# Optimization experiments

Measured on AMD Instinct MI355X. Metric: run time of the kernel, lower is better.

Reference implementation:

```python
import jax, jax.numpy as jnp
import numpy as np

B, SEQ, C, H, L = 2, 512, 768, 12, 6
OBS = ACT = GOAL = 64
MAXEP = 1000
D = C // H
T3 = 3 * SEQ  # stacked (z, state, action) tokens per timestep


def _ln(x, g, b):
    m = jnp.mean(x, -1, keepdims=True)
    v = jnp.mean((x - m) ** 2, -1, keepdims=True)
    return (x - m) * jax.lax.rsqrt(v + 1e-5) * g + b


def setup_inputs() -> dict:
    key = jax.random.key(0)
    it = iter(jax.random.split(key, 64))
    nrm = lambda shape, s=0.02: jax.random.normal(next(it), shape, jnp.float32) * s
    z = lambda *s: jnp.zeros(s, jnp.float32)
    o = lambda *s: jnp.ones(s, jnp.float32)
    return dict(
        states=jax.random.normal(next(it), (B, SEQ, OBS), jnp.float32),
        actions=jax.random.normal(next(it), (B, SEQ, ACT), jnp.float32),
        goals=jax.random.normal(next(it), (B, 1, GOAL), jnp.float32),
        traj_mask=jnp.ones((B, SEQ), bool),
        timesteps=jax.random.randint(next(it), (B, SEQ), 0, MAXEP),
        W_s=nrm((OBS, C)), b_s=z(C),
        W_a=nrm((ACT, C)), b_a=z(C),
        W_g=nrm((GOAL, C)), b_g=z(C),
        E_t=nrm((MAXEP, C)),
        ln0_g=o(C), ln0_b=z(C),
        Wq=nrm((L, C, C)), bq=z(L, C),
        Wk=nrm((L, C, C)), bk=z(L, C),
        Wv=nrm((L, C, C)), bv=z(L, C),
        Wp=nrm((L, C, C)), bp=z(L, C),
        ln1_g=o(L, C), ln1_b=z(L, C),
        W1=nrm((L, C, 4 * C)), b1=z(L, 4 * C),
        W2=nrm((L, 4 * C, C)), b2=z(L, C),
        ln2_g=o(L, C), ln2_b=z(L, C),
        W_ps=nrm((C, OBS)), b_ps=z(OBS),
        W_pa=nrm((C, ACT)), b_pa=z(ACT),
    )


def _forward(states, actions, goals, timesteps,
             W_s, b_s, W_a, b_a, W_g, b_g, E_t, ln0_g, ln0_b,
             Wq, bq, Wk, bk, Wv, bv, Wp, bp, ln1_g, ln1_b,
             W1, b1, W2, b2, ln2_g, ln2_b, W_ps, b_ps, W_pa, b_pa):
    te = E_t[timesteps]  # [B,SEQ,C] time embeddings (use_pe_as_timestep path)
    s_emb = states @ W_s + b_s + te
    a_emb = actions @ W_a + b_a + te
    g = jnp.broadcast_to(goals, (goals.shape[0], SEQ, goals.shape[2]))
    z_emb = g @ W_g + b_g + te  # GOAL_CONDITION path
    # interleave (z, s, a) per timestep -> [B, 3*SEQ, C]
    x = jnp.stack((z_emb, s_emb, a_emb), axis=2).reshape(states.shape[0], T3, C)
    x = _ln(x, ln0_g, ln0_b)
    mask = jnp.tril(jnp.ones((T3, T3), bool))
    scale = 1.0 / np.sqrt(D)
    for l in range(L):
        q = (x @ Wq[l] + bq[l]).reshape(-1, T3, H, D)
        k = (x @ Wk[l] + bk[l]).reshape(-1, T3, H, D)
        v = (x @ Wv[l] + bv[l]).reshape(-1, T3, H, D)
        sc = jnp.einsum('bqhd,bkhd->bhqk', q, k) * scale
        sc = jnp.where(mask, sc, -jnp.inf)
        w = jax.nn.softmax(sc, axis=-1)
        att = jnp.einsum('bhqk,bkhd->bqhd', w, v).reshape(-1, T3, C)
        x = x + att @ Wp[l] + bp[l]
        x = _ln(x, ln1_g[l], ln1_b[l])
        h = jax.nn.gelu(x @ W1[l] + b1[l], approximate=False)
        x = x + h @ W2[l] + b2[l]
        x = _ln(x, ln2_g[l], ln2_b[l])
    x = x.reshape(-1, SEQ, 3, C)
    state_preds = x[:, :, 2] @ W_ps + b_ps     # read off action-token positions
    action_preds = jnp.tanh(x[:, :, 1] @ W_pa + b_pa)  # state-token positions
    return jnp.stack((state_preds, action_preds))  # [2,B,SEQ,64]


def reference(states, actions, goals, traj_mask, timesteps,
              W_s, b_s, W_a, b_a, W_g, b_g, E_t, ln0_g, ln0_b,
              Wq, bq, Wk, bk, Wv, bv, Wp, bp, ln1_g, ln1_b,
              W1, b1, W2, b2, ln2_g, ln2_b, W_ps, b_ps, W_pa, b_pa):
    del traj_mask  # unused on the GOAL_CONDITION path
    return _forward(states, actions, goals, timesteps,
                    W_s, b_s, W_a, b_a, W_g, b_g, E_t, ln0_g, ln0_b,
                    Wq, bq, Wk, bk, Wv, bv, Wp, bp, ln1_g, ln1_b,
                    W1, b1, W2, b2, ln2_g, ln2_b, W_ps, b_ps, W_pa, b_pa)
```

## Files before the change

kernel.cpp:

```cpp
#include <hip/hip_runtime.h>

#define SEQ 512
#define T3 1536
#define CDIM 768
#define NH 12
#define HD 64
#define NL 6

typedef __attribute__((ext_vector_type(8))) short bh8;
typedef __attribute__((ext_vector_type(4))) short s4;
typedef __attribute__((ext_vector_type(4))) float f4;

__device__ inline short f2bf(float f) {
    union { float f; unsigned u; } x; x.f = f;
    unsigned r = x.u + 0x7FFFu + ((x.u >> 16) & 1u);
    return (short)(r >> 16);
}

__device__ inline float bf2f(short s) {
    union { unsigned u; float f; } x;
    x.u = ((unsigned)(unsigned short)s) << 16;
    return x.f;
}

__device__ inline void gload16(const short* g, const short* l) {
    __builtin_amdgcn_global_load_lds(
        (const __attribute__((address_space(1))) unsigned int*)g,
        (__attribute__((address_space(3))) unsigned int*)l, 16, 0, 0);
}

__device__ inline float block_sum(float v, volatile float* red, int tid) {
    #pragma unroll
    for (int off = 32; off > 0; off >>= 1) v += __shfl_down(v, off, 64);
    __syncthreads();
    if ((tid & 63) == 0) red[tid >> 6] = v;
    __syncthreads();
    return red[0] + red[1] + red[2] + red[3];
}

__global__ __launch_bounds__(256) void conv64_k(
        const float* __restrict__ Wq, const float* __restrict__ Wk,
        const float* __restrict__ Wv, const float* __restrict__ Wp,
        const float* __restrict__ W1, const float* __restrict__ W2,
        short* __restrict__ dst, int l0) {
    __shared__ float t2[2][64][65];
    int tid = threadIdx.x;
    int rk = tid >> 4, cn4 = (tid & 15) * 4;
    const float* srcA[2]; short* dA[2]; int KA[2], k0A[2], n0A[2];
    f4 vv[2][4];
    #pragma unroll
    for (int i = 0; i < 2; ++i) {
        int tt = blockIdx.x * 2 + i;
        int lrel = tt / 1728, r = tt - lrel * 1728;
        int l = l0 + lrel;
        short* dstL = dst + (size_t)lrel * 7077888;
        const float* src; short* d; int K, N, tk, tn;
        if (r < 576) {
            int mat = r / 144, t = r - mat * 144;
            tk = t / 12; tn = t % 12; K = 768; N = 768;
            const float* srcs[4] = {Wq, Wk, Wv, Wp};
            src = srcs[mat] + (size_t)l * 589824;
            d = dstL + mat * 589824;
        } else if (r < 1152) {
            int t = r - 576; tk = t / 48; tn = t % 48; K = 768; N = 3072;
            src = W1 + (size_t)l * 2359296; d = dstL + 2359296;
        } else {
            int t = r - 1152; tk = t / 12; tn = t % 12; K = 3072; N = 768;
            src = W2 + (size_t)l * 2359296; d = dstL + 4718592;
        }
        int k0 = tk * 64, n0 = tn * 64;
        srcA[i] = src; dA[i] = d; KA[i] = K; k0A[i] = k0; n0A[i] = n0;
        #pragma unroll
        for (int p = 0; p < 4; ++p)
            vv[i][p] = *(const f4*)(src + (size_t)(k0 + p * 16 + rk) * N + n0 + cn4);
    }
    #pragma unroll
    for (int i = 0; i < 2; ++i)
    #pragma unroll
    for (int p = 0; p < 4; ++p) {
        t2[i][cn4][p * 16 + rk]     = vv[i][p][0];
        t2[i][cn4 + 1][p * 16 + rk] = vv[i][p][1];
        t2[i][cn4 + 2][p * 16 + rk] = vv[i][p][2];
        t2[i][cn4 + 3][p * 16 + rk] = vv[i][p][3];
    }
    __syncthreads();
    int n = tid >> 2, kb = (tid & 3) * 16;
    #pragma unroll
    for (int i = 0; i < 2; ++i) {
        f4 a0 = *(const f4*)&t2[i][n][kb];
        f4 a1 = *(const f4*)&t2[i][n][kb + 4];
        f4 a2 = *(const f4*)&t2[i][n][kb + 8];
        f4 a3 = *(const f4*)&t2[i][n][kb + 12];
        bh8 o0, o1;
        o0[0] = f2bf(a0[0]); o0[1] = f2bf(a0[1]); o0[2] = f2bf(a0[2]); o0[3] = f2bf(a0[3]);
        o0[4] = f2bf(a1[0]); o0[5] = f2bf(a1[1]); o0[6] = f2bf(a1[2]); o0[7] = f2bf(a1[3]);
        o1[0] = f2bf(a2[0]); o1[1] = f2bf(a2[1]); o1[2] = f2bf(a2[2]); o1[3] = f2bf(a2[3]);
        o1[4] = f2bf(a3[0]); o1[5] = f2bf(a3[1]); o1[6] = f2bf(a3[2]); o1[7] = f2bf(a3[3]);
        short* wp = dA[i] + (size_t)(n0A[i] + n) * KA[i] + k0A[i] + kb;
        *(bh8*)wp = o0;
        *(bh8*)(wp + 8) = o1;
    }
}

__global__ __launch_bounds__(256) void embed_ln0_k(
        const float* __restrict__ states, const float* __restrict__ actions,
        const float* __restrict__ goals, const int* __restrict__ timesteps,
        const float* __restrict__ W_s, const float* __restrict__ b_s,
        const float* __restrict__ W_a, const float* __restrict__ b_a,
        const float* __restrict__ W_g, const float* __restrict__ b_g,
        const float* __restrict__ E_t, const float* __restrict__ g0,
        const float* __restrict__ bb0, float* __restrict__ x, short* __restrict__ xb) {
    int row = blockIdx.x;
    int b = row / T3, t3 = row - b * T3;
    int t = t3 / 3, kind = t3 - t * 3;
    __shared__ float inv[64];
    __shared__ float xr[CDIM];
    __shared__ float red[4];
    int tid = threadIdx.x;
    const float* src; const float* W; const float* bias;
    if (kind == 0)      { src = goals + b * 64;                       W = W_g; bias = b_g; }
    else if (kind == 1) { src = states + ((size_t)b * SEQ + t) * 64;  W = W_s; bias = b_s; }
    else                { src = actions + ((size_t)b * SEQ + t) * 64; W = W_a; bias = b_a; }
    if (tid < 64) inv[tid] = src[tid];
    __syncthreads();
    int ts = timesteps[b * SEQ + t];
    for (int c = tid; c < CDIM; c += 256) {
        float acc = bias[c] + E_t[(size_t)ts * CDIM + c];
        #pragma unroll 8
        for (int kk = 0; kk < 64; ++kk) acc += inv[kk] * W[kk * CDIM + c];
        xr[c] = acc;
    }
    __syncthreads();
    float v0 = xr[tid], v1 = xr[tid + 256], v2 = xr[tid + 512];
    float mean = block_sum(v0 + v1 + v2, red, tid) * (1.f / CDIM);
    float d0 = v0 - mean, d1 = v1 - mean, d2 = v2 - mean;
    float var = block_sum(d0 * d0 + d1 * d1 + d2 * d2, red, tid) * (1.f / CDIM);
    float rs = rsqrtf(var + 1e-5f);
    float* w = x + (size_t)row * CDIM;
    short* wb = xb + (size_t)row * CDIM;
    float o0 = d0 * rs * g0[tid]       + bb0[tid];
    float o1 = d1 * rs * g0[tid + 256] + bb0[tid + 256];
    float o2 = d2 * rs * g0[tid + 512] + bb0[tid + 512];
    w[tid] = o0; w[tid + 256] = o1; w[tid + 512] = o2;
    wb[tid] = f2bf(o0); wb[tid + 256] = f2bf(o1); wb[tid + 512] = f2bf(o2);
}

__global__ __launch_bounds__(256) void ln_k(float* __restrict__ x, short* __restrict__ outb,
                                            const float* __restrict__ g, const float* __restrict__ bb) {
    int wave = threadIdx.x >> 6, lane = threadIdx.x & 63;
    int row = blockIdx.x * 4 + wave;
    float* r = x + (size_t)row * CDIM;
    short* wb = outb + (size_t)row * CDIM;
    float v[12];
    float s = 0.f, s2 = 0.f;
    #pragma unroll
    for (int j = 0; j < 12; ++j) {
        v[j] = r[lane + j * 64];
        s += v[j]; s2 += v[j] * v[j];
    }
    #pragma unroll
    for (int off = 32; off > 0; off >>= 1) { s += __shfl_xor(s, off, 64); s2 += __shfl_xor(s2, off, 64); }
    float mean = s * (1.f / CDIM);
    float var = s2 * (1.f / CDIM) - mean * mean;
    float rs = rsqrtf(var + 1e-5f);
    #pragma unroll
    for (int j = 0; j < 12; ++j) {
        int c = lane + j * 64;
        float o = (v[j] - mean) * rs * g[c] + bb[c];
        r[c] = o;
        wb[c] = f2bf(o);
    }
}

template<int BM, int BN, int EPI, int DB>
__global__ __launch_bounds__(256) void gemm6_k(
        const short* __restrict__ A, const short* __restrict__ B0,
        const short* __restrict__ B1, const short* __restrict__ B2,
        const float* __restrict__ bias0, const float* __restrict__ bias1,
        const float* __restrict__ bias2,
        float* __restrict__ outF, short* __restrict__ outQ,
        short* __restrict__ outK, short* __restrict__ outV,
        int N, int K) {
    const short* Bw = B0; const float* bias = bias0; short* outB = outQ;
    int zid = 0;
    if (EPI == 0) {
        zid = blockIdx.z;
        if (zid == 1) { Bw = B1; bias = bias1; outB = outK; }
        else if (zid == 2) { Bw = B2; bias = bias2; outB = outV; }
    }
    __shared__ short As[(DB ? 2 : 1) * BM * 64];
    __shared__ short Bs[(DB ? 2 : 1) * BN * 64];
    int tid = threadIdx.x, lane = tid & 63, wave = tid >> 6;
    int wm = wave >> 1, wn = wave & 1, lr = lane & 15, lg = lane >> 4;
    int bm = blockIdx.y * BM, bn = blockIdx.x * BN;
    int rl = lane >> 3, ch = (lane & 7) ^ rl;
    constexpr int MI = BM / 32, NI = BN / 32;
    f4 acc[MI][NI] = {};

    auto STAGE = [&](int k0, int buf) {
        #pragma unroll
        for (int j = 0; j < BM / 32; ++j)
            gload16(A + (size_t)(bm + wave * (BM / 4) + j * 8 + rl) * K + k0 + ch * 8,
                    As + buf * BM * 64 + (wave * (BM / 4) + j * 8) * 64);
        #pragma unroll
        for (int j = 0; j < BN / 32; ++j)
            gload16(Bw + (size_t)(bn + wave * (BN / 4) + j * 8 + rl) * K + k0 + ch * 8,
                    Bs + buf * BN * 64 + (wave * (BN / 4) + j * 8) * 64);
    };

    auto COMPUTE = [&](int buf) {
        bh8 af[MI][2], bf[NI][2];
        #pragma unroll
        for (int mi = 0; mi < MI; ++mi)
        #pragma unroll
        for (int kk = 0; kk < 2; ++kk) {
            int m = wm * (BM / 2) + mi * 16 + lr;
            af[mi][kk] = *(const bh8*)(As + buf * BM * 64 + m * 64 + (((kk * 4 + lg) ^ (lr & 7)) * 8));
        }
        #pragma unroll
        for (int ni = 0; ni < NI; ++ni)
        #pragma unroll
        for (int kk = 0; kk < 2; ++kk) {
            int n = wn * (BN / 2) + ni * 16 + lr;
            bf[ni][kk] = *(const bh8*)(Bs + buf * BN * 64 + n * 64 + (((kk * 4 + lg) ^ (lr & 7)) * 8));
        }
        #pragma unroll
        for (int kk = 0; kk < 2; ++kk)
        #pragma unroll
        for (int mi = 0; mi < MI; ++mi)
        #pragma unroll
        for (int ni = 0; ni < NI; ++ni)
            acc[mi][ni] = __builtin_amdgcn_mfma_f32_16x16x32_bf16(af[mi][kk], bf[ni][kk], acc[mi][ni], 0, 0, 0);
    };

    if (DB) {
        STAGE(0, 0);
        int cur = 0;
        for (int k0 = 0; k0 < K; k0 += 64) {
            if (k0 + 64 < K) {
                STAGE(k0 + 64, cur ^ 1);
                asm volatile("s_waitcnt vmcnt(4)" ::: "memory");
            } else {
                asm volatile("s_waitcnt vmcnt(0)" ::: "memory");
            }
            __builtin_amdgcn_s_barrier();
            __builtin_amdgcn_sched_barrier(0);
            COMPUTE(cur);
            __builtin_amdgcn_sched_barrier(0);
            __builtin_amdgcn_s_barrier();
            cur ^= 1;
        }
    } else {
        for (int k0 = 0; k0 < K; k0 += 64) {
            STAGE(k0, 0);
            __syncthreads();
            COMPUTE(0);
            __syncthreads();
        }
    }

    #pragma unroll
    for (int mi = 0; mi < MI; ++mi)
    #pragma unroll
    for (int ni = 0; ni < NI; ++ni)
    #pragma unroll
    for (int i = 0; i < 4; ++i) {
        int row = bm + wm * (BM / 2) + mi * 16 + lg * 4 + i;
        int col = bn + wn * (BN / 2) + ni * 16 + lr;
        float vv = acc[mi][ni][i] + bias[col];
        if (EPI == 0) {
            int b = row / T3, t = row - b * T3;
            int h = col >> 6, d = col & 63;
            if (zid == 2) outB[((size_t)(b * NH + h) * 64 + d) * T3 + t] = f2bf(vv);
            else          outB[((((size_t)b * NH + h) * T3 + t) << 6) + d] = f2bf(vv);
        } else if (EPI == 1) {
            size_t idx = (size_t)row * N + col;
            outF[idx] = vv + outF[idx];
        } else {
            float gl = 0.5f * vv * (1.0f + erff(vv * 0.70710678118f));
            outQ[(size_t)row * N + col] = f2bf(gl);
        }
    }
}

__global__ __launch_bounds__(256) void attn_k(const short* __restrict__ q, const short* __restrict__ k,
                                              const short* __restrict__ vt, short* __restrict__ att) {
    int idx = blockIdx.x;
    int qt = 23 - (idx / 24);
    int bh = idx % 24;
    int b = bh / NH, h = bh - b * NH;
    const short* qb = q  + (size_t)bh * T3 * HD;
    const short* kb = k  + (size_t)bh * T3 * HD;
    const short* vb = vt + (size_t)bh * HD * T3;
    __shared__ short Ks[2][4096];
    __shared__ short Vs[2][4096];
    __shared__ short Pl[4][16][72];
    int tid = threadIdx.x, lane = tid & 63, wave = tid >> 6;
    int lr = lane & 15, lg = lane >> 4;
    int rl = lane >> 3, ch = (lane & 7) ^ rl;
    int qrow0 = qt * 64 + wave * 16;
    bh8 aq0 = *(const bh8*)(qb + (size_t)(qrow0 + lr) * HD + lg * 8);
    bh8 aq1 = *(const bh8*)(qb + (size_t)(qrow0 + lr) * HD + 32 + lg * 8);
    f4 o[4] = {};
    float lsum[4] = {0.f, 0.f, 0.f, 0.f};

    auto STAGE = [&](int kt2, int buf) {
        const short* kb2 = kb + (size_t)kt2 * 64 * HD;
        #pragma unroll
        for (int j = 0; j < 2; ++j)
            gload16(kb2 + (wave * 16 + j * 8 + rl) * HD + ch * 8,
                    &Ks[buf][(wave * 16 + j * 8) * 64]);
        const short* vb2 = vb + kt2 * 64;
        #pragma unroll
        for (int j = 0; j < 2; ++j)
            gload16(vb2 + (size_t)(wave * 16 + j * 8 + rl) * T3 + ch * 8,
                    &Vs[buf][(wave * 16 + j * 8) * 64]);
    };

    STAGE(0, 0);
    int cur = 0;
    for (int kt = 0; kt <= qt; ++kt) {
        if (kt < qt) {
            STAGE(kt + 1, cur ^ 1);
            asm volatile("s_waitcnt vmcnt(4)" ::: "memory");
        } else {
            asm volatile("s_waitcnt vmcnt(0)" ::: "memory");
        }
        __builtin_amdgcn_s_barrier();
        __builtin_amdgcn_sched_barrier(0);
        const short* Kb = &Ks[cur][0];
        const short* Vb = &Vs[cur][0];
        f4 s[4];
        #pragma unroll
        for (int nf = 0; nf < 4; ++nf) {
            int tok = nf * 16 + lr;
            bh8 bk0 = *(const bh8*)(Kb + tok * 64 + ((lg ^ (lr & 7)) * 8));
            bh8 bk1 = *(const bh8*)(Kb + tok * 64 + (((4 + lg) ^ (lr & 7)) * 8));
            f4 t = {};
            t = __builtin_amdgcn_mfma_f32_16x16x32_bf16(aq0, bk0, t, 0, 0, 0);
            t = __builtin_amdgcn_mfma_f32_16x16x32_bf16(aq1, bk1, t, 0, 0, 0);
            s[nf] = t;
        }
        #pragma unroll
        for (int nf = 0; nf < 4; ++nf)
        #pragma unroll
        for (int i = 0; i < 4; ++i) {
            float p = __expf(s[nf][i] * 0.125f);
            if (kt == qt && (nf * 16 + lr) > (wave * 16 + lg * 4 + i)) p = 0.f;
            lsum[i] += p;
            Pl[wave][lg * 4 + i][nf * 16 + lr] = f2bf(p);
        }
        bh8 ap0 = *(const bh8*)&Pl[wave][lr][lg * 8];
        bh8 ap1 = *(const bh8*)&Pl[wave][lr][32 + lg * 8];
        #pragma unroll
        for (int nf = 0; nf < 4; ++nf) {
            int d = nf * 16 + lr;
            bh8 bv0 = *(const bh8*)(Vb + d * 64 + ((lg ^ (lr & 7)) * 8));
            bh8 bv1 = *(const bh8*)(Vb + d * 64 + (((4 + lg) ^ (lr & 7)) * 8));
            o[nf] = __builtin_amdgcn_mfma_f32_16x16x32_bf16(ap0, bv0, o[nf], 0, 0, 0);
            o[nf] = __builtin_amdgcn_mfma_f32_16x16x32_bf16(ap1, bv1, o[nf], 0, 0, 0);
        }
        __builtin_amdgcn_sched_barrier(0);
        __builtin_amdgcn_s_barrier();
        cur ^= 1;
    }
    float linv[4];
    #pragma unroll
    for (int i = 0; i < 4; ++i) {
        float l = lsum[i];
        #pragma unroll
        for (int off = 1; off < 16; off <<= 1) l += __shfl_xor(l, off, 16);
        linv[i] = 1.f / l;
    }
    #pragma unroll
    for (int nf = 0; nf < 4; ++nf)
    #pragma unroll
    for (int i = 0; i < 4; ++i) {
        int qrow = qrow0 + lg * 4 + i;
        att[((size_t)b * T3 + qrow) * CDIM + h * 64 + nf * 16 + lr] = f2bf(o[nf][i] * linv[i]);
    }
}

__global__ __launch_bounds__(64) void head_k(const short* __restrict__ x,
                                             const float* __restrict__ Wps, const float* __restrict__ bps,
                                             const float* __restrict__ Wpa, const float* __restrict__ bpa,
                                             float* __restrict__ out) {
    int o = blockIdx.y;
    int bs = blockIdx.x;
    int b = bs >> 9, t = bs & 511;
    int kind = (o == 0) ? 2 : 1;
    const float* W = (o == 0) ? Wps : Wpa;
    const float* bi = (o == 0) ? bps : bpa;
    const short* xr = x + ((size_t)b * T3 + t * 3 + kind) * CDIM;
    int n = threadIdx.x;
    float a0 = 0.f, a1 = 0.f, a2 = 0.f, a3 = 0.f;
    for (int kk = 0; kk < CDIM; kk += 4) {
        s4 xv = *(const s4*)(xr + kk);
        a0 = fmaf(bf2f(xv[0]), W[(kk)     * 64 + n], a0);
        a1 = fmaf(bf2f(xv[1]), W[(kk + 1) * 64 + n], a1);
        a2 = fmaf(bf2f(xv[2]), W[(kk + 2) * 64 + n], a2);
        a3 = fmaf(bf2f(xv[3]), W[(kk + 3) * 64 + n], a3);
    }
    float acc = bi[n] + ((a0 + a1) + (a2 + a3));
    if (o == 1) acc = tanhf(acc);
    out[(((size_t)o * 2 + b) * SEQ + t) * 64 + n] = acc;
}

extern "C" void kernel_launch(void* const* d_in, const int* in_sizes, int n_in,
                              void* d_out, int out_size, void* d_ws, size_t ws_size,
                              hipStream_t stream) {
    const float* states    = (const float*)d_in[0];
    const float* actions   = (const float*)d_in[1];
    const float* goals     = (const float*)d_in[2];
    const int*   timesteps = (const int*)d_in[4];
    const float* W_s = (const float*)d_in[5];  const float* b_s = (const float*)d_in[6];
    const float* W_a = (const float*)d_in[7];  const float* b_a = (const float*)d_in[8];
    const float* W_g = (const float*)d_in[9];  const float* b_g = (const float*)d_in[10];
    const float* E_t = (const float*)d_in[11];
    const float* ln0_g = (const float*)d_in[12]; const float* ln0_b = (const float*)d_in[13];
    const float* Wq = (const float*)d_in[14]; const float* bq = (const float*)d_in[15];
    const float* Wk = (const float*)d_in[16]; const float* bk = (const float*)d_in[17];
    const float* Wv = (const float*)d_in[18]; const float* bv = (const float*)d_in[19];
    const float* Wp = (const float*)d_in[20]; const float* bp = (const float*)d_in[21];
    const float* ln1_g = (const float*)d_in[22]; const float* ln1_b = (const float*)d_in[23];
    const float* W1 = (const float*)d_in[24]; const float* b1 = (const float*)d_in[25];
    const float* W2 = (const float*)d_in[26]; const float* b2 = (const float*)d_in[27];
    const float* ln2_g = (const float*)d_in[28]; const float* ln2_b = (const float*)d_in[29];
    const float* W_ps = (const float*)d_in[30]; const float* b_ps = (const float*)d_in[31];
    const float* W_pa = (const float*)d_in[32]; const float* b_pa = (const float*)d_in[33];

    char* ws = (char*)d_ws;
    float* x_f   = (float*)(ws);
    short* x_bf  = (short*)(ws + 9437184);
    short* h_bf  = (short*)(ws + 14155776);
    short* qb    = (short*)(ws + 14155776);
    short* kb    = (short*)(ws + 18874368);
    short* vbt   = (short*)(ws + 23592960);
    short* wts   = (short*)(ws + 33030144);

    const long long WL = 7077888;
    bool allw = ws_size >= 117964800ull;

    embed_ln0_k<<<dim3(2 * T3), 256, 0, stream>>>(states, actions, goals, timesteps,
        W_s, b_s, W_a, b_a, W_g, b_g, E_t, ln0_g, ln0_b, x_f, x_bf);

    if (allw)
        conv64_k<<<dim3(1728 * NL / 2), 256, 0, stream>>>(Wq, Wk, Wv, Wp, W1, W2, wts, 0);

    for (int l = 0; l < NL; ++l) {
        size_t bo = (size_t)l * CDIM, b1o = (size_t)l * 4 * CDIM;
        if (!allw)
            conv64_k<<<dim3(1728 / 2), 256, 0, stream>>>(Wq, Wk, Wv, Wp, W1, W2, wts, l);
        short* wb  = wts + (allw ? (long long)l * WL : 0);
        short* Wqt = wb;
        short* Wkt = wb + 589824;
        short* Wvt = wb + 1179648;
        short* Wpt = wb + 1769472;
        short* W1t = wb + 2359296;
        short* W2t = wb + 4718592;

        gemm6_k<64, 64, 0, 1><<<dim3(12, 48, 3), 256, 0, stream>>>(x_bf, Wqt, Wkt, Wvt,
            bq + bo, bk + bo, bv + bo, nullptr, qb, kb, vbt, CDIM, CDIM);
        attn_k<<<dim3(576), 256, 0, stream>>>(qb, kb, vbt, x_bf);
        gemm6_k<64, 64, 1, 1><<<dim3(12, 48, 1), 256, 0, stream>>>(x_bf, Wpt, nullptr, nullptr,
            bp + bo, nullptr, nullptr, x_f, nullptr, nullptr, nullptr, CDIM, CDIM);
        ln_k<<<dim3(768), 256, 0, stream>>>(x_f, x_bf, ln1_g + bo, ln1_b + bo);
        gemm6_k<128, 64, 2, 0><<<dim3(48, 24, 1), 256, 0, stream>>>(x_bf, W1t, nullptr, nullptr,
            b1 + b1o, nullptr, nullptr, nullptr, h_bf, nullptr, nullptr, 4 * CDIM, CDIM);
        gemm6_k<64, 64, 1, 1><<<dim3(12, 48, 1), 256, 0, stream>>>(h_bf, W2t, nullptr, nullptr,
            b2 + bo, nullptr, nullptr, x_f, nullptr, nullptr, nullptr, CDIM, 4 * CDIM);
        ln_k<<<dim3(768), 256, 0, stream>>>(x_f, x_bf, ln2_g + bo, ln2_b + bo);
    }

    head_k<<<dim3(1024, 2), 64, 0, stream>>>(x_bf, W_ps, b_ps, W_pa, b_pa, (float*)d_out);
}
```

Before: 1.074 ms.

## Fuse LayerNorm into residual GEMM epilogue via last-block row-tile counters

The projection and second MLP GEMMs now count finished blocks per row tile with an atomic counter. The last block to finish a row tile runs the LayerNorm for those 64 rows, writing both the fp32 residual and the bf16 copy. This replaces the separate ln_k launches and the extra pass over the residual that came with them. The counters are reset by the attention kernel and the W1 GEMM, and the path is only taken when the workspace is large enough. In exchange, the LayerNorm for each row tile runs serially on a single block at the tail of the GEMM, and the change adds threadfence and atomic overhead.

```diff
diff --git a/kernel.cpp b/kernel.cpp
--- a/kernel.cpp
+++ b/kernel.cpp
@@ -172,7 +172,7 @@
     }
 }
 
-template<int BM, int BN, int EPI, int DB>
+template<int BM, int BN, int EPI, int DB, int FLN>
 __global__ __launch_bounds__(256) void gemm6_k(
         const short* __restrict__ A, const short* __restrict__ B0,
         const short* __restrict__ B1, const short* __restrict__ B2,
@@ -180,7 +180,11 @@
         const float* __restrict__ bias2,
         float* __restrict__ outF, short* __restrict__ outQ,
         short* __restrict__ outK, short* __restrict__ outV,
-        int N, int K) {
+        int N, int K,
+        const float* __restrict__ lnG, const float* __restrict__ lnB,
+        short* __restrict__ lnOut, int* cnt, int* cntZ) {
+    if (EPI == 2 && cntZ != nullptr && blockIdx.x == 0 && blockIdx.y == 0 && threadIdx.x < 48)
+        cntZ[threadIdx.x] = 0;
     const short* Bw = B0; const float* bias = bias0; short* outB = outQ;
     int zid = 0;
     if (EPI == 0) {
@@ -281,11 +285,54 @@
             outQ[(size_t)row * N + col] = f2bf(gl);
         }
     }
+
+    if (FLN) {
+        __threadfence();
+        __syncthreads();
+        __shared__ int lastF;
+        if (tid == 0) {
+            int old = atomicAdd(&cnt[blockIdx.y], 1);
+            lastF = (old == (int)gridDim.x - 1) ? 1 : 0;
+        }
+        __syncthreads();
+        if (lastF) {
+            __threadfence();
+            int wv2 = tid >> 6, l2 = tid & 63;
+            for (int rr = wv2; rr < BM; rr += 4) {
+                int row = blockIdx.y * BM + rr;
+                float* rp = outF + (size_t)row * CDIM;
+                short* wp2 = lnOut + (size_t)row * CDIM;
+                float vv2[12];
+                float s = 0.f, s2 = 0.f;
+                #pragma unroll
+                for (int j = 0; j < 12; ++j) {
+                    vv2[j] = rp[l2 + j * 64];
+                    s += vv2[j]; s2 += vv2[j] * vv2[j];
+                }
+                #pragma unroll
+                for (int off = 32; off > 0; off >>= 1) {
+                    s += __shfl_xor(s, off, 64); s2 += __shfl_xor(s2, off, 64);
+                }
+                float mean = s * (1.f / CDIM);
+                float var = s2 * (1.f / CDIM) - mean * mean;
+                float rs = rsqrtf(var + 1e-5f);
+                #pragma unroll
+                for (int j = 0; j < 12; ++j) {
+                    int c = l2 + j * 64;
+                    float oo = (vv2[j] - mean) * rs * lnG[c] + lnB[c];
+                    rp[c] = oo;
+                    wp2[c] = f2bf(oo);
+                }
+            }
+        }
+    }
 }
 
 __global__ __launch_bounds__(256) void attn_k(const short* __restrict__ q, const short* __restrict__ k,
-                                              const short* __restrict__ vt, short* __restrict__ att) {
+                                              const short* __restrict__ vt, short* __restrict__ att,
+                                              int* cntZ) {
     int idx = blockIdx.x;
+    if (cntZ != nullptr && idx == 0 && threadIdx.x < 48) cntZ[threadIdx.x] = 0;
     int qt = 23 - (idx / 24);
     int bh = idx % 24;
     int b = bh / NH, h = bh - b * NH;
@@ -440,6 +487,9 @@
 
     const long long WL = 7077888;
     bool allw = ws_size >= 117964800ull;
+    size_t cntOff = allw ? 117964800ull : 47185920ull;
+    bool fuseLN = ws_size >= cntOff + 256;
+    int* cnt = fuseLN ? (int*)(ws + cntOff) : nullptr;
 
     embed_ln0_k<<<dim3(2 * T3), 256, 0, stream>>>(states, actions, goals, timesteps,
         W_s, b_s, W_a, b_a, W_g, b_g, E_t, ln0_g, ln0_b, x_f, x_bf);
@@ -459,17 +509,33 @@
         short* W1t = wb + 2359296;
         short* W2t = wb + 4718592;
 
-        gemm6_k<64, 64, 0, 1><<<dim3(12, 48, 3), 256, 0, stream>>>(x_bf, Wqt, Wkt, Wvt,
-            bq + bo, bk + bo, bv + bo, nullptr, qb, kb, vbt, CDIM, CDIM);
-        attn_k<<<dim3(576), 256, 0, stream>>>(qb, kb, vbt, x_bf);
-        gemm6_k<64, 64, 1, 1><<<dim3(12, 48, 1), 256, 0, stream>>>(x_bf, Wpt, nullptr, nullptr,
-            bp + bo, nullptr, nullptr, x_f, nullptr, nullptr, nullptr, CDIM, CDIM);
-        ln_k<<<dim3(768), 256, 0, stream>>>(x_f, x_bf, ln1_g + bo, ln1_b + bo);
-        gemm6_k<128, 64, 2, 0><<<dim3(48, 24, 1), 256, 0, stream>>>(x_bf, W1t, nullptr, nullptr,
-            b1 + b1o, nullptr, nullptr, nullptr, h_bf, nullptr, nullptr, 4 * CDIM, CDIM);
-        gemm6_k<64, 64, 1, 1><<<dim3(12, 48, 1), 256, 0, stream>>>(h_bf, W2t, nullptr, nullptr,
-            b2 + bo, nullptr, nullptr, x_f, nullptr, nullptr, nullptr, CDIM, 4 * CDIM);
-        ln_k<<<dim3(768), 256, 0, stream>>>(x_f, x_bf, ln2_g + bo, ln2_b + bo);
+        gemm6_k<64, 64, 0, 1, 0><<<dim3(12, 48, 3), 256, 0, stream>>>(x_bf, Wqt, Wkt, Wvt,
+            bq + bo, bk + bo, bv + bo, nullptr, qb, kb, vbt, CDIM, CDIM,
+            nullptr, nullptr, nullptr, nullptr, nullptr);
+        attn_k<<<dim3(576), 256, 0, stream>>>(qb, kb, vbt, x_bf, cnt);
+        if (fuseLN) {
+            gemm6_k<64, 64, 1, 1, 1><<<dim3(12, 48, 1), 256, 0, stream>>>(x_bf, Wpt, nullptr, nullptr,
+                bp + bo, nullptr, nullptr, x_f, nullptr, nullptr, nullptr, CDIM, CDIM,
+                ln1_g + bo, ln1_b + bo, x_bf, cnt, nullptr);
+            gemm6_k<128, 64, 2, 0, 0><<<dim3(48, 24, 1), 256, 0, stream>>>(x_bf, W1t, nullptr, nullptr,
+                b1 + b1o, nullptr, nullptr, nullptr, h_bf, nullptr, nullptr, 4 * CDIM, CDIM,
+                nullptr, nullptr, nullptr, nullptr, cnt);
+            gemm6_k<64, 64, 1, 1, 1><<<dim3(12, 48, 1), 256, 0, stream>>>(h_bf, W2t, nullptr, nullptr,
+                b2 + bo, nullptr, nullptr, x_f, nullptr, nullptr, nullptr, CDIM, 4 * CDIM,
+                ln2_g + bo, ln2_b + bo, x_bf, cnt, nullptr);
+        } else {
+            gemm6_k<64, 64, 1, 1, 0><<<dim3(12, 48, 1), 256, 0, stream>>>(x_bf, Wpt, nullptr, nullptr,
+                bp + bo, nullptr, nullptr, x_f, nullptr, nullptr, nullptr, CDIM, CDIM,
+                nullptr, nullptr, nullptr, nullptr, nullptr);
+            ln_k<<<dim3(768), 256, 0, stream>>>(x_f, x_bf, ln1_g + bo, ln1_b + bo);
+            gemm6_k<128, 64, 2, 0, 0><<<dim3(48, 24, 1), 256, 0, stream>>>(x_bf, W1t, nullptr, nullptr,
+                b1 + b1o, nullptr, nullptr, nullptr, h_bf, nullptr, nullptr, 4 * CDIM, CDIM,
+                nullptr, nullptr, nullptr, nullptr, nullptr);
+            gemm6_k<64, 64, 1, 1, 0><<<dim3(12, 48, 1), 256, 0, stream>>>(h_bf, W2t, nullptr, nullptr,
+                b2 + bo, nullptr, nullptr, x_f, nullptr, nullptr, nullptr, CDIM, 4 * CDIM,
+                nullptr, nullptr, nullptr, nullptr, nullptr);
+            ln_k<<<dim3(768), 256, 0, stream>>>(x_f, x_bf, ln2_g + bo, ln2_b + bo);
+        }
     }
 
     head_k<<<dim3(1024, 2), 64, 0, stream>>>(x_bf, W_ps, b_ps, W_pa, b_pa, (float*)d_out);
```

Measured after the change: 2.148 ms. 2x slower.
